# Kernel optimization log

Measured on AMD Instinct MI355X. Metric: run time of the kernel, lower is better.

The kernel has to match this reference:

```python
import jax, jax.numpy as jnp
import numpy as np

D_MODEL = 128
N_HEADS = 8
D_K = D_MODEL // N_HEADS
N_NODES = 50000
N_EDGES = 800000


def setup_inputs() -> dict:
    key = jax.random.key(0)
    ks = jax.random.split(key, 8)
    X = jax.random.normal(ks[0], (N_NODES, D_MODEL), dtype=jnp.float32)
    nbr_src = jax.random.randint(ks[1], (N_EDGES,), 0, N_NODES, dtype=jnp.int32)
    nbr_dst = jax.random.randint(ks[2], (N_EDGES,), 0, N_NODES, dtype=jnp.int32)
    s = 1.0 / np.sqrt(D_MODEL)
    W_qkv = jax.random.normal(ks[3], (3 * D_MODEL, D_MODEL), dtype=jnp.float32) * s
    w_bias = jax.random.normal(ks[4], (N_HEADS, D_MODEL), dtype=jnp.float32) * s
    W_gate = jax.random.normal(ks[5], (D_MODEL, D_MODEL), dtype=jnp.float32) * s
    b_gate = jax.random.normal(ks[6], (D_MODEL,), dtype=jnp.float32) * s
    W_o = jax.random.normal(ks[7], (D_MODEL, D_MODEL), dtype=jnp.float32) * s
    return {"X": X, "W_qkv": W_qkv, "w_bias": w_bias, "W_gate": W_gate,
            "b_gate": b_gate, "W_o": W_o, "nbr_src": nbr_src,
            "nbr_dst": nbr_dst, "num_cells": N_NODES}


def segment_softmax(scores, seg, num_segments):
    # scores: [E, H], seg: [E] -> softmax over edges sharing the same seg id
    mx = jax.ops.segment_max(scores, seg, num_segments=num_segments)  # [N, H]
    mx = jnp.where(jnp.isfinite(mx), mx, -1e9)
    exp_s = jnp.exp(scores - mx[seg])
    sm = jax.ops.segment_sum(exp_s, seg, num_segments=num_segments)  # [N, H]
    return exp_s / (sm[seg] + 1e-12)


def reference(X, W_qkv, w_bias, W_gate, b_gate, W_o, nbr_src, nbr_dst, num_cells):
    H, dk = N_HEADS, D_K
    scale = 1.0 / np.sqrt(dk)
    qkv = (X @ W_qkv.T).reshape(-1, 3, H, dk)      # [N, 3, H, dk]
    Q, K, V = qkv[:, 0], qkv[:, 1], qkv[:, 2]
    gate = jax.nn.sigmoid(X @ W_gate.T + b_gate).reshape(-1, H, dk)
    bias = X @ w_bias.T                             # [N, H]
    scores = jnp.einsum('ehd,ehd->eh', Q[nbr_src], K[nbr_dst]) * scale + bias[nbr_src]
    attn = segment_softmax(scores, nbr_src, num_cells)          # [E, H]
    out = jax.ops.segment_sum(attn[:, :, None] * V[nbr_dst], nbr_src,
                              num_segments=num_cells)           # [N, H, dk]
    return (gate * out).reshape(-1, D_MODEL) @ W_o.T
```

## Files before the change

kernel.cpp:

```cpp
#include <hip/hip_runtime.h>
#include <hip/hip_fp16.h>

#define DM 128
#define NHEADS 8
#define MAXDEG 64
#define SROW 136

typedef _Float16 half8 __attribute__((ext_vector_type(8)));
typedef _Float16 half2v __attribute__((ext_vector_type(2)));
typedef float floatx4 __attribute__((ext_vector_type(4)));

union H8 { half8 v; half2v h2[4]; };

__global__ __launch_bounds__(256) void proj_csr(
    const float* __restrict__ X, const float* __restrict__ Wqkv,
    const float* __restrict__ Wgate, const float* __restrict__ wbias,
    const float* __restrict__ b_gate,
    const int* __restrict__ nsrc, const int* __restrict__ ndst,
    int* __restrict__ cnt, int* __restrict__ csr_dst,
    _Float16* __restrict__ Q, _Float16* __restrict__ KV,
    _Float16* __restrict__ gate, float* __restrict__ bias,
    int M, int E, int P) {
  __shared__ _Float16 As[128 * SROW];
  __shared__ _Float16 Bs[64 * SROW];
  int tid = threadIdx.x;
  int bid = blockIdx.x;

  if (bid >= P) {
    int ebase = (bid - P) * 8192;
    for (int g = 0; g < 4; g++) {
      int s[8], d[8];
#pragma unroll
      for (int j = 0; j < 8; j++) {
        int e = ebase + (g * 8 + j) * 256 + tid;
        s[j] = (e < E) ? nsrc[e] : -1;
        d[j] = (e < E) ? ndst[e] : 0;
      }
#pragma unroll
      for (int j = 0; j < 8; j++) {
        if (s[j] >= 0) {
          int p = atomicAdd(&cnt[s[j]], 1);
          if (p < MAXDEG) csr_dst[(size_t)s[j] * MAXDEG + p] = d[j];
        }
      }
    }
    return;
  }

  int m0 = bid * 128;

#pragma unroll
  for (int i = 0; i < 4; i++) {
    int u = tid + i * 256;
    int r = u >> 3;
    int cc = (u & 7) * 16;
    int gr = m0 + r;
    float4 f0, f1, f2, f3;
    if (gr < M) {
      const float4* src = (const float4*)(X + (size_t)gr * 128 + cc);
      f0 = src[0]; f1 = src[1]; f2 = src[2]; f3 = src[3];
    } else {
      f0 = f1 = f2 = f3 = make_float4(0.f, 0.f, 0.f, 0.f);
    }
    half8 h0 = {(_Float16)f0.x, (_Float16)f0.y, (_Float16)f0.z, (_Float16)f0.w,
                (_Float16)f1.x, (_Float16)f1.y, (_Float16)f1.z, (_Float16)f1.w};
    half8 h1 = {(_Float16)f2.x, (_Float16)f2.y, (_Float16)f2.z, (_Float16)f2.w,
                (_Float16)f3.x, (_Float16)f3.y, (_Float16)f3.z, (_Float16)f3.w};
    *(half8*)(As + r * SROW + cc) = h0;
    *(half8*)(As + r * SROW + cc + 8) = h1;
  }

  int wid = tid >> 6, lane = tid & 63;
  int quad = lane >> 4, l16 = lane & 15;
  int mw = wid * 32;

  for (int c = 0; c < 9; c++) {
    __syncthreads();
#pragma unroll
    for (int i = 0; i < 4; i++) {
      int u = tid + i * 256;
      int r = u >> 4;
      int cc = (u & 15) * 8;
      int grow = c * 64 + r;
      const float* src = nullptr;
      if (grow < 384)      src = Wqkv + (size_t)grow * 128 + cc;
      else if (grow < 512) src = Wgate + (size_t)(grow - 384) * 128 + cc;
      else if (grow < 520) src = wbias + (size_t)(grow - 512) * 128 + cc;
      half8 h = {};
      if (src) {
        float4 f0 = ((const float4*)src)[0];
        float4 f1 = ((const float4*)src)[1];
        h = half8{(_Float16)f0.x, (_Float16)f0.y, (_Float16)f0.z, (_Float16)f0.w,
                  (_Float16)f1.x, (_Float16)f1.y, (_Float16)f1.z, (_Float16)f1.w};
      }
      *(half8*)(Bs + r * SROW + cc) = h;
    }
    __syncthreads();

    floatx4 acc[2][4] = {};
#pragma unroll
    for (int kc = 0; kc < 4; kc++) {
      int ko = kc * 32 + quad * 8;
      half8 a0 = *(const half8*)(As + (mw + l16) * SROW + ko);
      half8 a1 = *(const half8*)(As + (mw + 16 + l16) * SROW + ko);
      half8 b[4];
#pragma unroll
      for (int ni = 0; ni < 4; ni++)
        b[ni] = *(const half8*)(Bs + (ni * 16 + l16) * SROW + ko);
#pragma unroll
      for (int ni = 0; ni < 4; ni++) {
        acc[0][ni] = __builtin_amdgcn_mfma_f32_16x16x32_f16(a0, b[ni], acc[0][ni], 0, 0, 0);
        acc[1][ni] = __builtin_amdgcn_mfma_f32_16x16x32_f16(a1, b[ni], acc[1][ni], 0, 0, 0);
      }
    }

    if (c == 8) {
      if (l16 < 8) {
#pragma unroll
        for (int mi = 0; mi < 2; mi++)
#pragma unroll
          for (int r = 0; r < 4; r++) {
            int row = m0 + mw + mi * 16 + quad * 4 + r;
            if (row < M) bias[(size_t)row * 8 + l16] = acc[mi][0][r];
          }
      }
    } else {
      int reg = c >> 1;
#pragma unroll
      for (int mi = 0; mi < 2; mi++) {
#pragma unroll
        for (int ni = 0; ni < 4; ni++) {
          int colL = (c & 1) * 64 + ni * 16 + l16;
#pragma unroll
          for (int r = 0; r < 4; r++) {
            int row = m0 + mw + mi * 16 + quad * 4 + r;
            if (row >= M) continue;
            float v = acc[mi][ni][r];
            if (reg == 0)      Q[(size_t)row * 128 + colL] = (_Float16)v;
            else if (reg == 1) KV[(size_t)row * 256 + colL] = (_Float16)v;
            else if (reg == 2) KV[(size_t)row * 256 + 128 + colL] = (_Float16)v;
            else gate[(size_t)row * 128 + colL] =
                   (_Float16)(1.0f / (1.0f + __expf(-(v + b_gate[colL]))));
          }
        }
      }
    }
  }
}

__global__ __launch_bounds__(256) void final_gemm_mfma(
    const _Float16* __restrict__ A, const float* __restrict__ Wo,
    float* __restrict__ C, int M) {
  __shared__ _Float16 As[128 * SROW];
  __shared__ _Float16 Bs[64 * SROW];
  int tid = threadIdx.x;
  int m0 = blockIdx.x * 128, n0 = blockIdx.y * 64;
#pragma unroll
  for (int i = 0; i < 8; i++) {
    int u = tid + i * 256;
    int r = u >> 4;
    int cc = (u & 15) * 8;
    int gr = m0 + r;
    int4 val = make_int4(0, 0, 0, 0);
    if (gr < M) val = *(const int4*)(A + (size_t)gr * 128 + cc);
    *(int4*)(As + r * SROW + cc) = val;
  }
#pragma unroll
  for (int i = 0; i < 4; i++) {
    int u = tid + i * 256;
    int r = u >> 4;
    int cc = (u & 15) * 8;
    const float* src = Wo + (size_t)(n0 + r) * 128 + cc;
    float4 f0 = ((const float4*)src)[0];
    float4 f1 = ((const float4*)src)[1];
    half8 h = {(_Float16)f0.x, (_Float16)f0.y, (_Float16)f0.z, (_Float16)f0.w,
               (_Float16)f1.x, (_Float16)f1.y, (_Float16)f1.z, (_Float16)f1.w};
    *(half8*)(Bs + r * SROW + cc) = h;
  }
  __syncthreads();

  int wid = tid >> 6, lane = tid & 63;
  int quad = lane >> 4, l16 = lane & 15;
  int mw = (wid >> 1) * 64;
  int nw = (wid & 1) * 32;

  floatx4 acc[4][2] = {};
#pragma unroll
  for (int kc = 0; kc < 4; kc++) {
    int ko = kc * 32 + quad * 8;
    half8 a[4], b[2];
#pragma unroll
    for (int mi = 0; mi < 4; mi++)
      a[mi] = *(const half8*)(As + (mw + mi * 16 + l16) * SROW + ko);
#pragma unroll
    for (int ni = 0; ni < 2; ni++)
      b[ni] = *(const half8*)(Bs + (nw + ni * 16 + l16) * SROW + ko);
#pragma unroll
    for (int mi = 0; mi < 4; mi++)
#pragma unroll
      for (int ni = 0; ni < 2; ni++)
        acc[mi][ni] = __builtin_amdgcn_mfma_f32_16x16x32_f16(a[mi], b[ni], acc[mi][ni], 0, 0, 0);
  }
#pragma unroll
  for (int mi = 0; mi < 4; mi++) {
#pragma unroll
    for (int ni = 0; ni < 2; ni++) {
      int col = n0 + nw + ni * 16 + l16;
#pragma unroll
      for (int r = 0; r < 4; r++) {
        int row = m0 + mw + mi * 16 + quad * 4 + r;
        if (row >= M) continue;
        C[(size_t)row * 128 + col] = acc[mi][ni][r];
      }
    }
  }
}

__global__ __launch_bounds__(256) void attn_fused(
    const int* __restrict__ cnt, const int* __restrict__ csr_dst,
    const _Float16* __restrict__ Q, const _Float16* __restrict__ KV,
    const float* __restrict__ bias, const _Float16* __restrict__ gate,
    _Float16* __restrict__ gated, int N) {
  int wave = threadIdx.x >> 6, lane = threadIdx.x & 63;
  int n = blockIdx.x * 4 + wave;
  if (n >= N) return;
  int deg = cnt[n];
  if (deg > MAXDEG) deg = MAXDEG;
  int qtr = lane >> 4, l16 = lane & 15;
  int ch0 = l16 * 8;

  int dstv = csr_dst[(size_t)n * MAXDEG + lane];

  H8 qu; qu.v = *(const half8*)(Q + (size_t)n * DM + ch0);
  float bias_h = bias[(size_t)n * NHEADS + (l16 >> 1)];

  float acc[8] = {};
  float den = 0.f;
  int iters = (deg + 3) >> 2;

  H8 k0, v0, k1, v1;
  k0.v = half8{}; v0.v = half8{}; k1.v = half8{}; v1.v = half8{};
  bool b0 = false, b1 = false;
  if (0 < iters) {
    int e = qtr;
    b0 = e < deg;
    int d = __shfl(dstv, e);
    d = b0 ? d : 0;
    const _Float16* kvp = KV + (size_t)d * 256 + ch0;
    k0.v = *(const half8*)kvp;
    v0.v = *(const half8*)(kvp + 128);
  }
  if (1 < iters) {
    int e = 4 + qtr;
    b1 = e < deg;
    int d = __shfl(dstv, e);
    d = b1 ? d : 0;
    const _Float16* kvp = KV + (size_t)d * 256 + ch0;
    k1.v = *(const half8*)kvp;
    v1.v = *(const half8*)(kvp + 128);
  }

  for (int it = 0; it < iters; it++) {
    H8 k2, v2;
    k2.v = half8{}; v2.v = half8{};
    bool b2 = false;
    if (it + 2 < iters) {
      int e = (it + 2) * 4 + qtr;
      b2 = e < deg;
      int d = __shfl(dstv, e);
      d = b2 ? d : 0;
      const _Float16* kvp = KV + (size_t)d * 256 + ch0;
      k2.v = *(const half8*)kvp;
      v2.v = *(const half8*)(kvp + 128);
    }
    float p = 0.f;
#pragma unroll
    for (int j = 0; j < 4; j++)
      p = __builtin_amdgcn_fdot2(qu.h2[j], k0.h2[j], p, false);
    p += __shfl_xor(p, 1);
    float w = __expf(p * 0.25f + bias_h);
    if (!b0) w = 0.f;
    den += w;
#pragma unroll
    for (int j = 0; j < 8; j++) acc[j] = fmaf(w, (float)v0.v[j], acc[j]);
    k0 = k1; v0 = v1; b0 = b1;
    k1 = k2; v1 = v2; b1 = b2;
  }
#pragma unroll
  for (int j = 0; j < 8; j++) acc[j] += __shfl_xor(acc[j], 16);
#pragma unroll
  for (int j = 0; j < 8; j++) acc[j] += __shfl_xor(acc[j], 32);
  den += __shfl_xor(den, 16);
  den += __shfl_xor(den, 32);

  if (qtr == 0) {
    float inv = 1.0f / (den + 1e-12f);
    half8 gv = *(const half8*)(gate + (size_t)n * DM + ch0);
    half8 o;
#pragma unroll
    for (int j = 0; j < 8; j++) o[j] = (_Float16)(acc[j] * inv * (float)gv[j]);
    *(half8*)(gated + (size_t)n * DM + ch0) = o;
  }
}

extern "C" void kernel_launch(void* const* d_in, const int* in_sizes, int n_in,
                              void* d_out, int out_size, void* d_ws, size_t ws_size,
                              hipStream_t stream) {
  const float* X     = (const float*)d_in[0];
  const float* Wqkv  = (const float*)d_in[1];
  const float* wbias = (const float*)d_in[2];
  const float* Wgate = (const float*)d_in[3];
  const float* bgate = (const float*)d_in[4];
  const float* Wo    = (const float*)d_in[5];
  const int*   nsrc  = (const int*)d_in[6];
  const int*   ndst  = (const int*)d_in[7];
  int N = in_sizes[0] / 128;
  int E = in_sizes[6];
  float* out = (float*)d_out;

  char* p = (char*)d_ws;
  _Float16* Q16     = (_Float16*)p; p += (size_t)N * 128 * sizeof(_Float16);
  _Float16* KV16    = (_Float16*)p; p += (size_t)N * 256 * sizeof(_Float16);
  _Float16* gate16  = (_Float16*)p; p += (size_t)N * 128 * sizeof(_Float16);
  _Float16* gated16 = (_Float16*)p; p += (size_t)N * 128 * sizeof(_Float16);
  float* bias       = (float*)p;    p += (size_t)N * 8 * sizeof(float);
  int* cnt          = (int*)p;      p += (size_t)N * sizeof(int);
  int* csr_dst      = (int*)p;      p += (size_t)N * MAXDEG * sizeof(int);

  hipMemsetAsync(cnt, 0, (size_t)N * sizeof(int), stream);

  int P = (N + 127) / 128;
  int C = (E + 8191) / 8192;
  proj_csr<<<P + C, 256, 0, stream>>>(X, Wqkv, Wgate, wbias, bgate, nsrc, ndst,
                                      cnt, csr_dst, Q16, KV16, gate16, bias, N, E, P);

  attn_fused<<<(N + 3) / 4, 256, 0, stream>>>(cnt, csr_dst, Q16, KV16, bias,
                                              gate16, gated16, N);

  dim3 fg((N + 127) / 128, 2);
  final_gemm_mfma<<<fg, 256, 0, stream>>>(gated16, Wo, out, N);
}
```

Before: 215.8 us.

## Split CSR build into own kernel, store 16-bit dst indices, prefetch weights

Moves the edge-to-CSR scatter out of the projection kernel into a separate launch with smaller per-block edge chunks. CSR destination indices are stored as unsigned 16-bit instead of 32-bit, halving the CSR footprint that attention gathers from. The projection GEMM now register-prefetches the next weight chunk while computing the current one. The 16-bit indices only work while node count is below 65536, and the extra launch serialises the CSR build after the GEMM instead of overlapping them.

```diff
diff --git a/kernel.cpp b/kernel.cpp
--- a/kernel.cpp
+++ b/kernel.cpp
@@ -12,42 +12,64 @@
 
 union H8 { half8 v; half2v h2[4]; };
 
-__global__ __launch_bounds__(256) void proj_csr(
+__global__ __launch_bounds__(256) void csr_build(
+    const int* __restrict__ nsrc, const int* __restrict__ ndst,
+    int* __restrict__ cnt, unsigned short* __restrict__ csr_dst, int E) {
+  int tid = threadIdx.x;
+  int ebase = blockIdx.x * 2048;
+  int s[8], d[8];
+#pragma unroll
+  for (int j = 0; j < 8; j++) {
+    int e = ebase + j * 256 + tid;
+    s[j] = (e < E) ? nsrc[e] : -1;
+    d[j] = (e < E) ? ndst[e] : 0;
+  }
+#pragma unroll
+  for (int j = 0; j < 8; j++) {
+    if (s[j] >= 0) {
+      int p = atomicAdd(&cnt[s[j]], 1);
+      if (p < MAXDEG) csr_dst[(size_t)s[j] * MAXDEG + p] = (unsigned short)d[j];
+    }
+  }
+}
+
+__device__ __forceinline__ void prefetch_B(
+    int tid, int c, const float* __restrict__ Wqkv,
+    const float* __restrict__ Wgate, const float* __restrict__ wbias,
+    float4 pf[4][2]) {
+#pragma unroll
+  for (int i = 0; i < 4; i++) {
+    int u = tid + i * 256;
+    int r = u >> 4;
+    int cc = (u & 15) * 8;
+    int grow = c * 64 + r;
+    const float* src = nullptr;
+    if (grow < 384)      src = Wqkv + (size_t)grow * 128 + cc;
+    else if (grow < 512) src = Wgate + (size_t)(grow - 384) * 128 + cc;
+    else if (grow < 520) src = wbias + (size_t)(grow - 512) * 128 + cc;
+    if (src) {
+      pf[i][0] = ((const float4*)src)[0];
+      pf[i][1] = ((const float4*)src)[1];
+    } else {
+      pf[i][0] = make_float4(0.f, 0.f, 0.f, 0.f);
+      pf[i][1] = make_float4(0.f, 0.f, 0.f, 0.f);
+    }
+  }
+}
+
+__global__ __launch_bounds__(256) void proj_gemm(
     const float* __restrict__ X, const float* __restrict__ Wqkv,
     const float* __restrict__ Wgate, const float* __restrict__ wbias,
     const float* __restrict__ b_gate,
-    const int* __restrict__ nsrc, const int* __restrict__ ndst,
-    int* __restrict__ cnt, int* __restrict__ csr_dst,
     _Float16* __restrict__ Q, _Float16* __restrict__ KV,
-    _Float16* __restrict__ gate, float* __restrict__ bias,
-    int M, int E, int P) {
+    _Float16* __restrict__ gate, float* __restrict__ bias, int M) {
   __shared__ _Float16 As[128 * SROW];
   __shared__ _Float16 Bs[64 * SROW];
   int tid = threadIdx.x;
-  int bid = blockIdx.x;
-
-  if (bid >= P) {
-    int ebase = (bid - P) * 8192;
-    for (int g = 0; g < 4; g++) {
-      int s[8], d[8];
-#pragma unroll
-      for (int j = 0; j < 8; j++) {
-        int e = ebase + (g * 8 + j) * 256 + tid;
-        s[j] = (e < E) ? nsrc[e] : -1;
-        d[j] = (e < E) ? ndst[e] : 0;
-      }
-#pragma unroll
-      for (int j = 0; j < 8; j++) {
-        if (s[j] >= 0) {
-          int p = atomicAdd(&cnt[s[j]], 1);
-          if (p < MAXDEG) csr_dst[(size_t)s[j] * MAXDEG + p] = d[j];
-        }
-      }
-    }
-    return;
-  }
-
-  int m0 = bid * 128;
+  int m0 = blockIdx.x * 128;
+
+  float4 pf[4][2];
+  prefetch_B(tid, 0, Wqkv, Wgate, wbias, pf);
 
 #pragma unroll
   for (int i = 0; i < 4; i++) {
@@ -81,20 +103,13 @@
       int u = tid + i * 256;
       int r = u >> 4;
       int cc = (u & 15) * 8;
-      int grow = c * 64 + r;
-      const float* src = nullptr;
-      if (grow < 384)      src = Wqkv + (size_t)grow * 128 + cc;
-      else if (grow < 512) src = Wgate + (size_t)(grow - 384) * 128 + cc;
-      else if (grow < 520) src = wbias + (size_t)(grow - 512) * 128 + cc;
-      half8 h = {};
-      if (src) {
-        float4 f0 = ((const float4*)src)[0];
-        float4 f1 = ((const float4*)src)[1];
-        h = half8{(_Float16)f0.x, (_Float16)f0.y, (_Float16)f0.z, (_Float16)f0.w,
-                  (_Float16)f1.x, (_Float16)f1.y, (_Float16)f1.z, (_Float16)f1.w};
-      }
+      half8 h = {(_Float16)pf[i][0].x, (_Float16)pf[i][0].y,
+                 (_Float16)pf[i][0].z, (_Float16)pf[i][0].w,
+                 (_Float16)pf[i][1].x, (_Float16)pf[i][1].y,
+                 (_Float16)pf[i][1].z, (_Float16)pf[i][1].w};
       *(half8*)(Bs + r * SROW + cc) = h;
     }
+    if (c < 8) prefetch_B(tid, c + 1, Wqkv, Wgate, wbias, pf);
     __syncthreads();
 
     floatx4 acc[2][4] = {};
@@ -217,7 +232,7 @@
 }
 
 __global__ __launch_bounds__(256) void attn_fused(
-    const int* __restrict__ cnt, const int* __restrict__ csr_dst,
+    const int* __restrict__ cnt, const unsigned short* __restrict__ csr_dst,
     const _Float16* __restrict__ Q, const _Float16* __restrict__ KV,
     const float* __restrict__ bias, const _Float16* __restrict__ gate,
     _Float16* __restrict__ gated, int N) {
@@ -325,14 +340,17 @@
   _Float16* gated16 = (_Float16*)p; p += (size_t)N * 128 * sizeof(_Float16);
   float* bias       = (float*)p;    p += (size_t)N * 8 * sizeof(float);
   int* cnt          = (int*)p;      p += (size_t)N * sizeof(int);
-  int* csr_dst      = (int*)p;      p += (size_t)N * MAXDEG * sizeof(int);
+  unsigned short* csr_dst = (unsigned short*)p;
+  p += (size_t)N * MAXDEG * sizeof(unsigned short);
 
   hipMemsetAsync(cnt, 0, (size_t)N * sizeof(int), stream);
 
   int P = (N + 127) / 128;
-  int C = (E + 8191) / 8192;
-  proj_csr<<<P + C, 256, 0, stream>>>(X, Wqkv, Wgate, wbias, bgate, nsrc, ndst,
-                                      cnt, csr_dst, Q16, KV16, gate16, bias, N, E, P);
+  proj_gemm<<<P, 256, 0, stream>>>(X, Wqkv, Wgate, wbias, bgate,
+                                   Q16, KV16, gate16, bias, N);
+
+  int C = (E + 2047) / 2048;
+  csr_build<<<C, 256, 0, stream>>>(nsrc, ndst, cnt, csr_dst, E);
 
   attn_fused<<<(N + 3) / 4, 256, 0, stream>>>(cnt, csr_dst, Q16, KV16, bias,
                                               gate16, gated16, N);
```

After: 250.8 us. +16.2%, slower.
